# Performance work log

Hardware: AMD Instinct MI355X
Metric: run time of the kernel (lower is better)

Reference implementation:

```python
import jax, jax.numpy as jnp
import numpy as np

TOP_K = 8
NUM_EXPERTS = 256
N_GROUP = 8
TOPK_GROUP = 4
SCALE = 2.5
RENORMALIZE = True
TOKENS = 131072


def setup_inputs() -> dict:
    key = jax.random.key(0)
    k1, k2 = jax.random.split(key)
    router_logits = jax.random.normal(k1, (TOKENS, NUM_EXPERTS), dtype=jnp.float32)
    expert_bias = jax.random.normal(k2, (NUM_EXPERTS,), dtype=jnp.float32) * 0.1
    return {"router_logits": router_logits, "expert_bias": expert_bias}


def _group_limited_topk(biased):
    # biased: [T, E]
    T = biased.shape[0]
    epg = NUM_EXPERTS // N_GROUP  # experts per group
    grouped = biased.reshape(T, N_GROUP, epg)
    # group score = sum of top-2 expert scores in each group
    top2_vals, _ = jax.lax.top_k(grouped, 2)
    group_scores = top2_vals.sum(axis=-1)  # [T, G]
    _, group_idx = jax.lax.top_k(group_scores, TOPK_GROUP)  # [T, Kg]
    group_mask = jnp.zeros((T, N_GROUP), dtype=bool).at[
        jnp.arange(T)[:, None], group_idx
    ].set(True)
    score_mask = jnp.repeat(group_mask, epg, axis=-1)  # [T, E]
    masked = jnp.where(score_mask, biased, -jnp.inf)
    _, topk_ids = jax.lax.top_k(masked, TOP_K)  # [T, K]
    return topk_ids


def reference(router_logits, expert_bias):
    scores = jax.nn.sigmoid(router_logits.astype(jnp.float32)).astype(router_logits.dtype)
    topk_ids = _group_limited_topk(scores + expert_bias)
    topk_weights = jnp.take_along_axis(scores, topk_ids, axis=-1)  # [T, K]
    if RENORMALIZE and TOP_K > 1:
        topk_weights = topk_weights / (topk_weights.sum(axis=-1, keepdims=True) + 1e-20)
    topk_weights = topk_weights * SCALE
    return topk_weights, topk_ids
```

## Files before the change

### kernel.cpp

```cpp
#include <hip/hip_runtime.h>
#include <math.h>


#define SWZF(x, mask) __int_as_float(__builtin_amdgcn_ds_swizzle(__float_as_int(x), (((mask) << 10) | 0x1F)))
#define SWZI(x, mask) __builtin_amdgcn_ds_swizzle((x), (((mask) << 10) | 0x1F))
#define DPPF(x, ctrl) __int_as_float(__builtin_amdgcn_update_dpp(__float_as_int(x), __float_as_int(x), (ctrl), 0xF, 0xF, true))
#define DPPI(x, ctrl) __builtin_amdgcn_update_dpp((x), (x), (ctrl), 0xF, 0xF, true)
#define QP_X1 0xB1
#define QP_X2 0x4E
#define QP_X3 0x1B

__global__ __launch_bounds__(256) void router_topk_kernel(
    const float* __restrict__ logits,
    const float* __restrict__ bias,
    float* __restrict__ out_w,
    float* __restrict__ out_id,
    int T)
{
    const float NEGINF = -__builtin_inff();
    const int tid  = threadIdx.x;
    const int lane = tid & 63;
    const int wid  = tid >> 6;
    const int s    = tid & 7;
    const int tw   = (tid >> 3) & 7;
    const int token = blockIdx.x * 32 + (tid >> 3);
    const int wtok0 = blockIdx.x * 32 + (wid << 3);

    __shared__ float4 xp[2048];
    float4* xw = xp + (wid << 9);

    {
        float4 gbuf[8];
        #pragma unroll
        for (int j = 0; j < 8; ++j) {
            int r = wtok0 + j;
            r = (r < T) ? r : (T - 1);
            gbuf[j] = ((const float4*)(logits + ((size_t)r << 8)))[lane];
        }
        #pragma unroll
        for (int j = 0; j < 8; ++j)
            xw[(j << 6) | (lane ^ j)] = gbuf[j];
    }

    const float* brw = bias + s * 32;
    float v[8][4];

    #pragma unroll
    for (int c = 0; c < 8; ++c) {
        float4 l = xw[(tw << 6) | (s << 3) | (c ^ tw)];
        float4 b = ((const float4*)brw)[c];
        #pragma unroll
        for (int k = 0; k < 4; ++k) {
            float x = (&l.x)[k];
            v[c][k] = 1.0f / (1.0f + expf(-x)) + (&b.x)[k];
        }
    }

    float t1 = NEGINF, t2 = NEGINF;
    #pragma unroll
    for (int c = 0; c < 8; ++c) {
        #pragma unroll
        for (int k = 0; k < 4; ++k) {
            float val = v[c][k];
            t2 = __builtin_amdgcn_fmed3f(t1, t2, val);
            t1 = fmaxf(t1, val);
        }
    }
    const float gs = t1 + t2;

    #pragma unroll
    for (int c = 0; c < 8; ++c)
        xw[(tw << 6) | (c << 3) | (s ^ tw)] = make_float4(v[c][0], v[c][1], v[c][2], v[c][3]);

    int rank = 0;
    {
        float g1 = DPPF(gs, QP_X1);
        float g2 = DPPF(gs, QP_X2);
        float g3 = DPPF(gs, QP_X3);
        float g4 = SWZF(gs, 4);
        float g5 = DPPF(g4, QP_X1);
        float g6 = DPPF(g4, QP_X2);
        float g7 = DPPF(g4, QP_X3);
        rank += (g1 > gs || (g1 == gs && (s & 1))) ? 1 : 0;
        rank += (g2 > gs || (g2 == gs && (s & 2))) ? 1 : 0;
        rank += (g3 > gs || (g3 == gs && (s & 2))) ? 1 : 0;
        rank += (g4 > gs || (g4 == gs && (s & 4))) ? 1 : 0;
        rank += (g5 > gs || (g5 == gs && (s & 4))) ? 1 : 0;
        rank += (g6 > gs || (g6 == gs && (s & 4))) ? 1 : 0;
        rank += (g7 > gs || (g7 == gs && (s & 4))) ? 1 : 0;
    }
    const bool selected = rank < 4;

    int msk = selected ? (1 << s) : 0;
    msk |= DPPI(msk, QP_X1);
    msk |= DPPI(msk, QP_X2);
    msk |= SWZI(msk, 4);

    unsigned m0 = (unsigned)msk;
    int g0 = __builtin_ctz(m0);
    unsigned m1 = m0 & (m0 - 1);
    int g1 = __builtin_ctz(m1);
    unsigned m2 = m1 & (m1 - 1);
    int g2 = __builtin_ctz(m2);
    unsigned m3 = m2 & (m2 - 1);
    int g3 = __builtin_ctz(m3);
    int ga = (s & 2) ? g1 : g0;
    int gb = (s & 2) ? g3 : g2;
    const int grp = (s & 4) ? gb : ga;
    const int h4  = (s & 1) << 2;

    float    f[4][4];
    unsigned pix[4];
    {
        const int rb = (tw << 6) | (grp ^ tw);
        #pragma unroll
        for (int j = 0; j < 4; ++j) {
            float4 nb = xw[rb | ((h4 + j) << 3)];
            f[j][0] = nb.x; f[j][1] = nb.y; f[j][2] = nb.z; f[j][3] = nb.w;
        }
        const unsigned ebase = (unsigned)(grp * 32 + (h4 << 2));
        const unsigned pbase = ebase * 0x01010101u;
        pix[0] = pbase + 0x03020100u;
        pix[1] = pbase + 0x07060504u;
        pix[2] = pbase + 0x0B0A0908u;
        pix[3] = pbase + 0x0F0E0D0Cu;
    }

    #pragma unroll
    for (int c = 0; c < 4; ++c) {
        #define CE(A, B, KM) { \
            unsigned p  = pix[c]; \
            unsigned ia = (p >> (8*(A))) & 0xFFu; \
            unsigned ib = (p >> (8*(B))) & 0xFFu; \
            bool sw = (f[c][A] < f[c][B]) || (f[c][A] == f[c][B] && ia > ib); \
            float hv = sw ? f[c][B] : f[c][A]; \
            float lv = sw ? f[c][A] : f[c][B]; \
            f[c][A] = hv; f[c][B] = lv; \
            unsigned ps = (p & (KM)) | (ia << (8*(B))) | (ib << (8*(A))); \
            pix[c] = sw ? ps : p; \
        }
        CE(0,1,0xFFFF0000u) CE(2,3,0x0000FFFFu)
        CE(0,2,0xFF00FF00u) CE(1,3,0x00FF00FFu) CE(1,2,0xFF0000FFu)
        #undef CE
    }

    float keepV = 0.0f; int keepI = 0;
    #pragma unroll
    for (int r = 0; r < 8; ++r) {
        const int h0 = (int)(pix[0] & 0xFFu);
        const int h1 = (int)(pix[1] & 0xFFu);
        const int h2 = (int)(pix[2] & 0xFFu);
        const int h3 = (int)(pix[3] & 0xFFu);
        float w0v, w1v, bv; int w0i, w1i, bi;
        { bool t = (f[1][0] > f[0][0]); w0v = t ? f[1][0] : f[0][0]; w0i = t ? h1 : h0; }
        { bool t = (f[3][0] > f[2][0]); w1v = t ? f[3][0] : f[2][0]; w1i = t ? h3 : h2; }
        { bool t = (w1v > w0v);         bv  = t ? w1v : w0v;         bi  = t ? w1i : w0i; }
        { float ov = DPPF(bv, QP_X1); int oi = DPPI(bi, QP_X1);
          bool t = (ov > bv) || (ov == bv && oi < bi); bv = t ? ov : bv; bi = t ? oi : bi; }
        { float ov = DPPF(bv, QP_X2); int oi = DPPI(bi, QP_X2);
          bool t = (ov > bv) || (ov == bv && oi < bi); bv = t ? ov : bv; bi = t ? oi : bi; }
        { float ov = SWZF(bv, 4);     int oi = SWZI(bi, 4);
          bool t = (ov > bv) || (ov == bv && oi < bi); bv = t ? ov : bv; bi = t ? oi : bi; }
        if (s == r) { keepV = bv; keepI = bi; }
        {
            bool hit = (h0 == bi);
            f[0][0] = hit ? f[0][1] : f[0][0];
            f[0][1] = hit ? f[0][2] : f[0][1];
            f[0][2] = hit ? f[0][3] : f[0][2];
            f[0][3] = hit ? NEGINF  : f[0][3];
            pix[0]  = hit ? (pix[0] >> 8) : pix[0];
        }
        {
            bool hit = (h1 == bi);
            f[1][0] = hit ? f[1][1] : f[1][0];
            f[1][1] = hit ? f[1][2] : f[1][1];
            f[1][2] = hit ? f[1][3] : f[1][2];
            f[1][3] = hit ? NEGINF  : f[1][3];
            pix[1]  = hit ? (pix[1] >> 8) : pix[1];
        }
        {
            bool hit = (h2 == bi);
            f[2][0] = hit ? f[2][1] : f[2][0];
            f[2][1] = hit ? f[2][2] : f[2][1];
            f[2][2] = hit ? f[2][3] : f[2][2];
            f[2][3] = hit ? NEGINF  : f[2][3];
            pix[2]  = hit ? (pix[2] >> 8) : pix[2];
        }
        {
            bool hit = (h3 == bi);
            f[3][0] = hit ? f[3][1] : f[3][0];
            f[3][1] = hit ? f[3][2] : f[3][1];
            f[3][2] = hit ? f[3][3] : f[3][2];
            f[3][3] = hit ? NEGINF  : f[3][3];
            pix[3]  = hit ? (pix[3] >> 8) : pix[3];
        }
    }

    float w = keepV - bias[keepI];
    float sum = w;
    sum += DPPF(sum, QP_X1);
    sum += DPPF(sum, QP_X2);
    sum += SWZF(sum, 4);
    w = w / (sum + 1e-20f) * 2.5f;

    if (token < T) {
        const size_t o = (size_t)blockIdx.x * 256 + tid;
        out_w[o]  = w;
        out_id[o] = (float)keepI;
    }
}

extern "C" void kernel_launch(void* const* d_in, const int* in_sizes, int n_in,
                              void* d_out, int out_size, void* d_ws, size_t ws_size,
                              hipStream_t stream) {
    const float* logits = (const float*)d_in[0];
    const float* bias   = (const float*)d_in[1];
    const int E = in_sizes[1];
    const int T = in_sizes[0] / E;
    float* out_w  = (float*)d_out;
    float* out_id = out_w + (size_t)T * 8;
    const int blocks = (T + 31) / 32;
    router_topk_kernel<<<blocks, 256, 0, stream>>>(logits, bias, out_w, out_id, T);
}
```

Measured before the change: 202.0 us.

## Load logits directly per thread and compact only selected groups into LDS

Drops the coalesced global-to-LDS staging of logits. Each thread now reads its 32 logits straight from global memory as float4s. Only the 4 selected groups per token are written to a smaller LDS buffer, with the group ids compacted through a popcount position, which removes the ctz-based group decode. This cuts LDS traffic and footprint, which may raise occupancy. The cost is that each thread strides across a row in global memory, so loads may be less coalesced, and an early return is added for out-of-range tokens.

```diff
diff --git a/kernel.cpp b/kernel.cpp
--- a/kernel.cpp
+++ b/kernel.cpp
@@ -19,35 +19,25 @@
 {
     const float NEGINF = -__builtin_inff();
     const int tid  = threadIdx.x;
-    const int lane = tid & 63;
     const int wid  = tid >> 6;
     const int s    = tid & 7;
     const int tw   = (tid >> 3) & 7;
     const int token = blockIdx.x * 32 + (tid >> 3);
-    const int wtok0 = blockIdx.x * 32 + (wid << 3);
-
-    __shared__ float4 xp[2048];
-    float4* xw = xp + (wid << 9);
-
-    {
-        float4 gbuf[8];
-        #pragma unroll
-        for (int j = 0; j < 8; ++j) {
-            int r = wtok0 + j;
-            r = (r < T) ? r : (T - 1);
-            gbuf[j] = ((const float4*)(logits + ((size_t)r << 8)))[lane];
-        }
-        #pragma unroll
-        for (int j = 0; j < 8; ++j)
-            xw[(j << 6) | (lane ^ j)] = gbuf[j];
-    }
-
+    if (token >= T) return;
+
+    __shared__ float4 cb[1024];
+    __shared__ int    gb[128];
+    float4* cw = cb + (wid << 8);
+    int*    gw = gb + (wid << 5);
+
+    const float* row = logits + (size_t)token * 256 + s * 32;
     const float* brw = bias + s * 32;
+
     float v[8][4];
 
     #pragma unroll
     for (int c = 0; c < 8; ++c) {
-        float4 l = xw[(tw << 6) | (s << 3) | (c ^ tw)];
+        float4 l = ((const float4*)row)[c];
         float4 b = ((const float4*)brw)[c];
         #pragma unroll
         for (int k = 0; k < 4; ++k) {
@@ -67,10 +57,6 @@
         }
     }
     const float gs = t1 + t2;
-
-    #pragma unroll
-    for (int c = 0; c < 8; ++c)
-        xw[(tw << 6) | (c << 3) | (s ^ tw)] = make_float4(v[c][0], v[c][1], v[c][2], v[c][3]);
 
     int rank = 0;
     {
@@ -96,26 +82,23 @@
     msk |= DPPI(msk, QP_X2);
     msk |= SWZI(msk, 4);
 
-    unsigned m0 = (unsigned)msk;
-    int g0 = __builtin_ctz(m0);
-    unsigned m1 = m0 & (m0 - 1);
-    int g1 = __builtin_ctz(m1);
-    unsigned m2 = m1 & (m1 - 1);
-    int g2 = __builtin_ctz(m2);
-    unsigned m3 = m2 & (m2 - 1);
-    int g3 = __builtin_ctz(m3);
-    int ga = (s & 2) ? g1 : g0;
-    int gb = (s & 2) ? g3 : g2;
-    const int grp = (s & 4) ? gb : ga;
+    if (selected) {
+        const int pos = __popc((unsigned)msk & ((1u << s) - 1u));
+        #pragma unroll
+        for (int c = 0; c < 8; ++c)
+            cw[(tw << 5) | (((c + tw) & 7) << 2) | pos] =
+                make_float4(v[c][0], v[c][1], v[c][2], v[c][3]);
+        gw[(tw << 2) | pos] = s;
+    }
+
     const int h4  = (s & 1) << 2;
-
+    const int grp = gw[(tw << 2) | (s >> 1)];
     float    f[4][4];
     unsigned pix[4];
     {
-        const int rb = (tw << 6) | (grp ^ tw);
         #pragma unroll
         for (int j = 0; j < 4; ++j) {
-            float4 nb = xw[rb | ((h4 + j) << 3)];
+            float4 nb = cw[(tw << 5) | ((((h4 + j) + tw) & 7) << 2) | (s >> 1)];
             f[j][0] = nb.x; f[j][1] = nb.y; f[j][2] = nb.z; f[j][3] = nb.w;
         }
         const unsigned ebase = (unsigned)(grp * 32 + (h4 << 2));
@@ -203,11 +186,9 @@
     sum += SWZF(sum, 4);
     w = w / (sum + 1e-20f) * 2.5f;
 
-    if (token < T) {
-        const size_t o = (size_t)blockIdx.x * 256 + tid;
-        out_w[o]  = w;
-        out_id[o] = (float)keepI;
-    }
+    const size_t o = (size_t)blockIdx.x * 256 + tid;
+    out_w[o]  = w;
+    out_id[o] = (float)keepI;
 }
 
 extern "C" void kernel_launch(void* const* d_in, const int* in_sizes, int n_in,
```

After: 203.8 us. No clear change (+0.9%).
